# Kernel tuning notes

Hardware: AMD Instinct MI355X
Metric: run time of the kernel (lower is better)

## Reference

```python
import jax, jax.numpy as jnp
import numpy as np

B = 131072      # flattened batch of item embeddings
E = 256         # e_dim; x has 2*E features (src half, rec half)
NQ = 4          # residual quantizer levels per branch
NE = 256        # codebook size per level
BETA = 0.25


def setup_inputs() -> dict:
    key = jax.random.key(0)
    k1, k2, k3 = jax.random.split(key, 3)
    x = jax.random.normal(k1, (B, 2 * E), dtype=jnp.float32)
    src_codebooks = jax.random.normal(k2, (NQ, NE, E), dtype=jnp.float32)
    rec_codebooks = jax.random.normal(k3, (NQ, NE, E), dtype=jnp.float32)
    return {"x": x, "src_codebooks": src_codebooks, "rec_codebooks": rec_codebooks}


def _vq(residual, cb):
    # residual: [B, E], cb: [NE, E]
    # squared euclidean distances via expanded form (GEMM-dominated)
    d = (jnp.sum(residual * residual, axis=1, keepdims=True)
         - 2.0 * (residual @ cb.T)
         + jnp.sum(cb * cb, axis=1)[None, :])          # [B, NE]
    idx = jnp.argmin(d, axis=1)                          # [B]
    x_q = cb[idx]                                        # gather [B, E]
    loss = (jnp.mean((jax.lax.stop_gradient(x_q) - residual) ** 2)
            + BETA * jnp.mean((x_q - jax.lax.stop_gradient(residual)) ** 2))
    # straight-through estimator
    x_q = residual + jax.lax.stop_gradient(x_q - residual)
    return x_q, loss, idx


def _rq(x_part, codebooks):
    # sequential residual VQ chain over NQ levels (small fixed unroll)
    residual = x_part
    x_q = jnp.zeros_like(x_part)
    losses, indices = [], []
    for i in range(codebooks.shape[0]):
        x_res, l, idx = _vq(residual, codebooks[i])
        residual = residual - x_res
        x_q = x_q + x_res
        losses.append(l)
        indices.append(idx)
    return x_q, jnp.stack(losses), jnp.stack(indices, axis=-1)


def reference(x, src_codebooks, rec_codebooks):
    src_x_q, src_l, src_idx = _rq(x[:, :E], src_codebooks)
    rec_x_q, rec_l, rec_idx = _rq(x[:, E:], rec_codebooks)
    mean_loss = jnp.mean(jnp.concatenate([src_l, rec_l]))
    return ((src_x_q, rec_x_q), mean_loss, (src_idx, rec_idx))
```

## Files before the change

### kernel.cpp

```cpp
#include <hip/hip_runtime.h>
#include <hip/hip_bf16.h>
#include <hip/hip_fp16.h>
#include <cstdint>
#include <cstddef>

#define NB   131072
#define ED   256
#define NQL  4
#define NEC  256

typedef _Float16 f16;
typedef f16  f16x8 __attribute__((ext_vector_type(8)));
typedef float f32x4 __attribute__((ext_vector_type(4)));

static constexpr float FMAXV = 3.402823466e+38f;
static constexpr float TAUH  = 0.078125f;

static constexpr size_t OFF_REC  = (size_t)NB * ED;
static constexpr size_t OFF_LOSS = 2 * (size_t)NB * ED;
static constexpr size_t OFF_SIDX = OFF_LOSS + 1;
static constexpr size_t OFF_RIDX = OFF_SIDX + (size_t)NB * NQL;

static constexpr size_t WS_LOSS = 0;
static constexpr size_t WS_NORM = 256;
static constexpr size_t WS_CBH  = 256 + 8 * 256 * 4;

__global__ void kPrep(const float* __restrict__ cbS, const float* __restrict__ cbR,
                      float* __restrict__ norms, double* __restrict__ lossAcc) {
  const int cbi = blockIdx.x;
  const int j   = threadIdx.x;
  if (cbi == 0 && j < 8) lossAcc[j] = 0.0;
  const float* row = (cbi < 4 ? cbS : cbR) + ((size_t)(cbi & 3) * NEC + j) * ED;
  float acc = 0.f;
  for (int k = 0; k < ED; k += 4) {
    float4 v = *(const float4*)(row + k);
    acc += v.x * v.x + v.y * v.y + v.z * v.z + v.w * v.w;
  }
  norms[cbi * NEC + j] = acc - 256.0f;
}

__global__ void kConvH(const float* __restrict__ cbS, const float* __restrict__ cbR,
                       f16* __restrict__ cbH) {
  const int f   = blockIdx.x * 256 + threadIdx.x;
  const int cbi = f >> 16;
  const int rem = f & 65535;
  const float v = (cbi < 4 ? cbS + ((size_t)cbi << 16) : cbR + ((size_t)(cbi - 4) << 16))[rem];
  cbH[f] = (f16)(-v);
}

__device__ __forceinline__ float pk(float v, int j) {
  return __uint_as_float((__float_as_uint(v) & ~255u) | (unsigned)j);
}
__device__ __forceinline__ float unpv(float k) {
  return __uint_as_float(__float_as_uint(k) & ~255u);
}
__device__ __forceinline__ void ins3(float& s0, float& s1, float& s2, float k) {
  float t0 = fmaxf(s0, k); s0 = fminf(s0, k);
  float t1 = fmaxf(s1, t0); s1 = fminf(s1, t0);
  s2 = fminf(s2, t1);
}
__device__ __forceinline__ void mrg3(float& a0, float& a1, float& a2,
                                     float b0, float b1, float b2) {
  float x  = fmaxf(a0, b0);
  float c0 = fminf(a0, b0);
  float m1 = fminf(a1, b1), M1 = fmaxf(a1, b1);
  float c1 = fminf(fminf(x, a1), b1);
  float c2 = fminf(fminf(fmaxf(x, m1), M1), fminf(a2, b2));
  a0 = c0; a1 = c1; a2 = c2;
}

__global__ __launch_bounds__(256, 2)
void kMain(const float* __restrict__ x,
           const float* __restrict__ cbS,
           const float* __restrict__ cbR,
           const f16*  __restrict__ cbH,
           const float* __restrict__ norms,
           double* __restrict__ lossAcc,
           float* __restrict__ out) {
  __shared__ __align__(16) char  RhBuf[64 * 512];
  __shared__ __align__(16) float keybuf[64][4][4];
  __shared__ float redS[4];

  const int tid   = threadIdx.x;
  const int lane  = tid & 63;
  const int w     = tid >> 6;
  const int it_o  = tid >> 2;
  const int kq    = tid & 3;
  const int b0    = blockIdx.x * 64;
  const int br    = blockIdx.y;
  const int l15   = lane & 15;
  const int l4    = lane >> 4;

  const float* cbf32base = br ? cbR : cbS;
  float res[64];
  float lossA = 0.f, lossB = 0.f, lossC = 0.f, lossD = 0.f;

  {
    const float* xp = x + (size_t)(b0 + it_o) * (2 * ED) + br * ED + kq * 64;
#pragma unroll
    for (int i = 0; i < 16; ++i) {
      float4 v = *(const float4*)(xp + 4 * i);
      res[4 * i + 0] = v.x; res[4 * i + 1] = v.y;
      res[4 * i + 2] = v.z; res[4 * i + 3] = v.w;
    }
  }

#pragma unroll 1
  for (int lev = 0; lev < NQL; ++lev) {
    const int cbi = br * 4 + lev;
    const float* nrm = norms + (size_t)cbi * NEC;
    const f16*   cbh = cbH + ((size_t)cbi << 16);
    const float* cbf32 = cbf32base + (size_t)lev * NEC * ED;

#pragma unroll
    for (int c = 0; c < 8; ++c) {
      f16x8 h;
#pragma unroll
      for (int u = 0; u < 8; ++u) h[u] = (f16)res[c * 8 + u];
      int off = it_o * 512 + kq * 128 + c * 16;
      off ^= (it_o & 7) << 4;
      *(f16x8*)&RhBuf[off] = h;
    }

    f32x4 acc[4][4];
#pragma unroll
    for (int nt = 0; nt < 4; ++nt) {
      float4 nv = *(const float4*)&nrm[w * 64 + nt * 16 + l4 * 4];
      f32x4 h; h[0] = 0.5f * nv.x; h[1] = 0.5f * nv.y;
      h[2] = 0.5f * nv.z; h[3] = 0.5f * nv.w;
#pragma unroll
      for (int mt = 0; mt < 4; ++mt) acc[mt][nt] = h;
    }

    f16x8 A0[4], B0[4], A1[4], B1[4];
#define LOADA(Adst, ks_)                                                        \
    {                                                                           \
      _Pragma("unroll")                                                         \
      for (int mt = 0; mt < 4; ++mt) {                                          \
        const int it = mt * 16 + l15;                                           \
        const int offA = (it * 512 + (ks_) * 64 + l4 * 16) ^ ((it & 7) << 4);   \
        Adst[mt] = *(const f16x8*)&RhBuf[offA];                                 \
      }                                                                         \
    }
#define LOADB(Bdst, ks_)                                                        \
    {                                                                           \
      _Pragma("unroll")                                                         \
      for (int nt = 0; nt < 4; ++nt) {                                          \
        const int j = w * 64 + nt * 16 + l15;                                   \
        Bdst[nt] = *(const f16x8*)&cbh[(size_t)j * ED + (ks_) * 32 + l4 * 8];   \
      }                                                                         \
    }
#define MFMA16(Aop, Bop)                                                        \
    {                                                                           \
      __builtin_amdgcn_s_setprio(1);                                            \
      _Pragma("unroll")                                                         \
      for (int mt = 0; mt < 4; ++mt)                                            \
        _Pragma("unroll")                                                       \
        for (int nt = 0; nt < 4; ++nt)                                          \
          acc[mt][nt] = __builtin_amdgcn_mfma_f32_16x16x32_f16(                 \
              Bop[nt], Aop[mt], acc[mt][nt], 0, 0, 0);                          \
      __builtin_amdgcn_s_setprio(0);                                            \
    }

    LOADB(B0, 0);
    __syncthreads();
    LOADA(A0, 0);
#pragma unroll 1
    for (int ks2 = 0; ks2 < 4; ++ks2) {
      LOADA(A1, 2 * ks2 + 1); LOADB(B1, 2 * ks2 + 1);
      MFMA16(A0, B0);
      if (ks2 < 3) { LOADA(A0, 2 * ks2 + 2); LOADB(B0, 2 * ks2 + 2); }
      MFMA16(A1, B1);
    }
#undef LOADA
#undef LOADB
#undef MFMA16

#pragma unroll
    for (int mt = 0; mt < 4; ++mt) {
      float s0 = FMAXV, s1 = FMAXV, s2 = FMAXV;
#pragma unroll
      for (int nt = 0; nt < 4; ++nt)
#pragma unroll
        for (int r = 0; r < 4; ++r)
          ins3(s0, s1, s2, pk(acc[mt][nt][r], w * 64 + nt * 16 + l4 * 4 + r));
      {
        float b0k = __shfl_xor(s0, 16), b1k = __shfl_xor(s1, 16), b2k = __shfl_xor(s2, 16);
        mrg3(s0, s1, s2, b0k, b1k, b2k);
        b0k = __shfl_xor(s0, 32); b1k = __shfl_xor(s1, 32); b2k = __shfl_xor(s2, 32);
        mrg3(s0, s1, s2, b0k, b1k, b2k);
      }
      if (l4 == 0) {
        float4 v; v.x = s0; v.y = s1; v.z = s2; v.w = FMAXV;
        *(float4*)&keybuf[mt * 16 + l15][w][0] = v;
      }
    }
    __syncthreads();

    int jm;
    {
      float4 v = *(const float4*)&keybuf[it_o][kq][0];
      float s0 = v.x, s1 = v.y, s2 = v.z;
      {
        float b0k = __shfl_xor(s0, 1), b1k = __shfl_xor(s1, 1), b2k = __shfl_xor(s2, 1);
        mrg3(s0, s1, s2, b0k, b1k, b2k);
        b0k = __shfl_xor(s0, 2); b1k = __shfl_xor(s1, 2); b2k = __shfl_xor(s2, 2);
        mrg3(s0, s1, s2, b0k, b1k, b2k);
      }
      jm = (int)(__float_as_uint(s0) & 255u);
      const float gap = unpv(s1) - unpv(s0);
      if (gap < TAUH) {
        const int cand[3] = { jm, (int)(__float_as_uint(s1) & 255u),
                                  (int)(__float_as_uint(s2) & 255u) };
        float bestd = FMAXV; int bestj = 0;
#pragma unroll 1
        for (int cc = 0; cc < 3; ++cc) {
          const int j = cand[cc];
          const float* row = cbf32 + (size_t)j * ED + kq * 64;
          float p2 = 0.f;
#pragma unroll
          for (int i = 0; i < 16; ++i) {
            float4 q = *(const float4*)(row + 4 * i);
            p2 = fmaf(res[4 * i + 0], q.x, p2);
            p2 = fmaf(res[4 * i + 1], q.y, p2);
            p2 = fmaf(res[4 * i + 2], q.z, p2);
            p2 = fmaf(res[4 * i + 3], q.w, p2);
          }
          p2 += __shfl_xor(p2, 1);
          p2 += __shfl_xor(p2, 2);
          const float d = fmaf(-2.f, p2, nrm[j]);
          if (d < bestd || (d == bestd && j < bestj)) { bestd = d; bestj = j; }
        }
        jm = bestj;
      }
      if (kq == 0) {
        const size_t ioff = (br ? OFF_RIDX : OFF_SIDX) + (size_t)(b0 + it_o) * NQL + lev;
        out[ioff] = (float)jm;
      }
    }

    {
      const float* crow = cbf32 + (size_t)jm * ED + kq * 64;
#pragma unroll
      for (int i = 0; i < 16; ++i) {
        float4 q = *(const float4*)(crow + 4 * i);
#pragma unroll
        for (int u = 0; u < 4; ++u) {
          float cv = (u == 0 ? q.x : u == 1 ? q.y : u == 2 ? q.z : q.w);
          float r  = res[4 * i + u];
          float dd = cv - r;
          if      (u == 0) lossA = fmaf(dd, dd, lossA);
          else if (u == 1) lossB = fmaf(dd, dd, lossB);
          else if (u == 2) lossC = fmaf(dd, dd, lossC);
          else             lossD = fmaf(dd, dd, lossD);
          float xr = r + dd;
          res[4 * i + u] = r - xr;
        }
      }
    }
  }

  {
    const float* xp = x + (size_t)(b0 + it_o) * (2 * ED) + br * ED + kq * 64;
    float* op = out + (br ? OFF_REC : 0) + (size_t)(b0 + it_o) * ED + kq * 64;
#pragma unroll
    for (int i = 0; i < 16; ++i) {
      float4 xv = *(const float4*)(xp + 4 * i);
      float4 o;
      o.x = xv.x - res[4 * i + 0];
      o.y = xv.y - res[4 * i + 1];
      o.z = xv.z - res[4 * i + 2];
      o.w = xv.w - res[4 * i + 3];
      *(float4*)(op + 4 * i) = o;
    }
  }

  float lossReg = (lossA + lossB) + (lossC + lossD);
#pragma unroll
  for (int d = 1; d < 64; d <<= 1) lossReg += __shfl_xor(lossReg, d);
  if (lane == 0) redS[w] = lossReg;
  __syncthreads();
  if (tid == 0)
    atomicAdd(&lossAcc[blockIdx.x & 7], (double)((redS[0] + redS[1]) + (redS[2] + redS[3])));
}

__global__ void kFin(const double* __restrict__ lossAcc, float* __restrict__ out) {
  if (blockIdx.x == 0 && threadIdx.x == 0) {
    double s = 0.0;
    for (int l = 0; l < 8; ++l) s += lossAcc[l];
    out[OFF_LOSS] = (float)(s * 1.25 / ((double)NB * ED) / 8.0);
  }
}

extern "C" void kernel_launch(void* const* d_in, const int* in_sizes, int n_in,
                              void* d_out, int out_size, void* d_ws, size_t ws_size,
                              hipStream_t stream) {
  const float* x   = (const float*)d_in[0];
  const float* cbS = (const float*)d_in[1];
  const float* cbR = (const float*)d_in[2];
  float* out = (float*)d_out;
  char*  ws  = (char*)d_ws;

  double* lossAcc = (double*)(ws + WS_LOSS);
  float*  norms   = (float*)(ws + WS_NORM);
  f16*    cbH     = (f16*)(ws + WS_CBH);

  hipLaunchKernelGGL(kPrep,  dim3(8),    dim3(256), 0, stream, cbS, cbR, norms, lossAcc);
  hipLaunchKernelGGL(kConvH, dim3(2048), dim3(256), 0, stream, cbS, cbR, cbH);
  hipLaunchKernelGGL(kMain,  dim3(NB / 64, 2), dim3(256), 0, stream,
                     x, cbS, cbR, cbH, norms, lossAcc, out);
  hipLaunchKernelGGL(kFin,   dim3(1),    dim3(64),  0, stream, lossAcc, out);
}
```

Measured before the change: 566.4 us.

## Fuse residual staging into update and prefetch next level's codebook tile

Converts the new residual to f16 and writes it to shared memory inside the residual-update loop, so the separate conversion pass per level goes away. The first B fragment of the next level's codebook is issued right after the argmin sync, so its latency overlaps the index refinement and update. The k-loop is fully unrolled. This adds register pressure and relies on the existing single __syncthreads per level to order the shared-memory writes before the next level's reads.

New measurement: 689.3 us. 21.7% more time.

```diff
diff --git a/kernel.cpp b/kernel.cpp
--- a/kernel.cpp
+++ b/kernel.cpp
@@ -95,44 +95,8 @@
   float res[64];
   float lossA = 0.f, lossB = 0.f, lossC = 0.f, lossD = 0.f;
 
-  {
-    const float* xp = x + (size_t)(b0 + it_o) * (2 * ED) + br * ED + kq * 64;
-#pragma unroll
-    for (int i = 0; i < 16; ++i) {
-      float4 v = *(const float4*)(xp + 4 * i);
-      res[4 * i + 0] = v.x; res[4 * i + 1] = v.y;
-      res[4 * i + 2] = v.z; res[4 * i + 3] = v.w;
-    }
-  }
-
-#pragma unroll 1
-  for (int lev = 0; lev < NQL; ++lev) {
-    const int cbi = br * 4 + lev;
-    const float* nrm = norms + (size_t)cbi * NEC;
-    const f16*   cbh = cbH + ((size_t)cbi << 16);
-    const float* cbf32 = cbf32base + (size_t)lev * NEC * ED;
-
-#pragma unroll
-    for (int c = 0; c < 8; ++c) {
-      f16x8 h;
-#pragma unroll
-      for (int u = 0; u < 8; ++u) h[u] = (f16)res[c * 8 + u];
-      int off = it_o * 512 + kq * 128 + c * 16;
-      off ^= (it_o & 7) << 4;
-      *(f16x8*)&RhBuf[off] = h;
-    }
-
-    f32x4 acc[4][4];
-#pragma unroll
-    for (int nt = 0; nt < 4; ++nt) {
-      float4 nv = *(const float4*)&nrm[w * 64 + nt * 16 + l4 * 4];
-      f32x4 h; h[0] = 0.5f * nv.x; h[1] = 0.5f * nv.y;
-      h[2] = 0.5f * nv.z; h[3] = 0.5f * nv.w;
-#pragma unroll
-      for (int mt = 0; mt < 4; ++mt) acc[mt][nt] = h;
-    }
-
-    f16x8 A0[4], B0[4], A1[4], B1[4];
+  f16x8 A0[4], A1[4], B0[4], B1[4];
+
 #define LOADA(Adst, ks_)                                                        \
     {                                                                           \
       _Pragma("unroll")                                                         \
@@ -142,12 +106,12 @@
         Adst[mt] = *(const f16x8*)&RhBuf[offA];                                 \
       }                                                                         \
     }
-#define LOADB(Bdst, ks_)                                                        \
+#define LOADB(Bdst, ks_, CBH_)                                                  \
     {                                                                           \
       _Pragma("unroll")                                                         \
       for (int nt = 0; nt < 4; ++nt) {                                          \
         const int j = w * 64 + nt * 16 + l15;                                   \
-        Bdst[nt] = *(const f16x8*)&cbh[(size_t)j * ED + (ks_) * 32 + l4 * 8];   \
+        Bdst[nt] = *(const f16x8*)&(CBH_)[(size_t)j * ED + (ks_) * 32 + l4 * 8];\
       }                                                                         \
     }
 #define MFMA16(Aop, Bop)                                                        \
@@ -162,19 +126,54 @@
       __builtin_amdgcn_s_setprio(0);                                            \
     }
 
-    LOADB(B0, 0);
+  {
+    const float* xp = x + (size_t)(b0 + it_o) * (2 * ED) + br * ED + kq * 64;
+#pragma unroll
+    for (int c = 0; c < 8; ++c) {
+      float4 v0 = *(const float4*)(xp + 8 * c);
+      float4 v1 = *(const float4*)(xp + 8 * c + 4);
+      res[8 * c + 0] = v0.x; res[8 * c + 1] = v0.y;
+      res[8 * c + 2] = v0.z; res[8 * c + 3] = v0.w;
+      res[8 * c + 4] = v1.x; res[8 * c + 5] = v1.y;
+      res[8 * c + 6] = v1.z; res[8 * c + 7] = v1.w;
+      f16x8 h;
+      h[0] = (f16)v0.x; h[1] = (f16)v0.y; h[2] = (f16)v0.z; h[3] = (f16)v0.w;
+      h[4] = (f16)v1.x; h[5] = (f16)v1.y; h[6] = (f16)v1.z; h[7] = (f16)v1.w;
+      const int off = (it_o * 512 + kq * 128 + c * 16) ^ ((it_o & 7) << 4);
+      *(f16x8*)&RhBuf[off] = h;
+    }
+  }
+  LOADB(B0, 0, cbH + ((size_t)(br * 4) << 16));
+
+#pragma unroll 1
+  for (int lev = 0; lev < NQL; ++lev) {
+    const int cbi = br * 4 + lev;
+    const float* nrm = norms + (size_t)cbi * NEC;
+    const f16*   cbh = cbH + ((size_t)cbi << 16);
+    const float* cbf32 = cbf32base + (size_t)lev * NEC * ED;
+    const bool doStage = (lev < 3);
+
+    f32x4 acc[4][4];
+#pragma unroll
+    for (int nt = 0; nt < 4; ++nt) {
+      float4 nv = *(const float4*)&nrm[w * 64 + nt * 16 + l4 * 4];
+      f32x4 h; h[0] = 0.5f * nv.x; h[1] = 0.5f * nv.y;
+      h[2] = 0.5f * nv.z; h[3] = 0.5f * nv.w;
+#pragma unroll
+      for (int mt = 0; mt < 4; ++mt) acc[mt][nt] = h;
+    }
+
     __syncthreads();
+
     LOADA(A0, 0);
-#pragma unroll 1
-    for (int ks2 = 0; ks2 < 4; ++ks2) {
-      LOADA(A1, 2 * ks2 + 1); LOADB(B1, 2 * ks2 + 1);
-      MFMA16(A0, B0);
-      if (ks2 < 3) { LOADA(A0, 2 * ks2 + 2); LOADB(B0, 2 * ks2 + 2); }
-      MFMA16(A1, B1);
-    }
-#undef LOADA
-#undef LOADB
-#undef MFMA16
+    LOADA(A1, 1); LOADB(B1, 1, cbh); MFMA16(A0, B0);
+    LOADA(A0, 2); LOADB(B0, 2, cbh); MFMA16(A1, B1);
+    LOADA(A1, 3); LOADB(B1, 3, cbh); MFMA16(A0, B0);
+    LOADA(A0, 4); LOADB(B0, 4, cbh); MFMA16(A1, B1);
+    LOADA(A1, 5); LOADB(B1, 5, cbh); MFMA16(A0, B0);
+    LOADA(A0, 6); LOADB(B0, 6, cbh); MFMA16(A1, B1);
+    LOADA(A1, 7); LOADB(B1, 7, cbh); MFMA16(A0, B0);
+    MFMA16(A1, B1);
 
 #pragma unroll
     for (int mt = 0; mt < 4; ++mt) {
@@ -196,6 +195,8 @@
       }
     }
     __syncthreads();
+
+    if (doStage) LOADB(B0, 0, cbh + (1 << 16));
 
     int jm;
     {
@@ -241,6 +242,7 @@
 
     {
       const float* crow = cbf32 + (size_t)jm * ED + kq * 64;
+      f16x8 h;
 #pragma unroll
       for (int i = 0; i < 16; ++i) {
         float4 q = *(const float4*)(crow + 4 * i);
@@ -254,11 +256,21 @@
           else if (u == 2) lossC = fmaf(dd, dd, lossC);
           else             lossD = fmaf(dd, dd, lossD);
           float xr = r + dd;
-          res[4 * i + u] = r - xr;
+          float rn = r - xr;
+          res[4 * i + u] = rn;
+          h[(i & 1) * 4 + u] = (f16)rn;
         }
-      }
-    }
-  }
+        if (doStage && (i & 1)) {
+          const int c = i >> 1;
+          const int off = (it_o * 512 + kq * 128 + c * 16) ^ ((it_o & 7) << 4);
+          *(f16x8*)&RhBuf[off] = h;
+        }
+      }
+    }
+  }
+#undef LOADA
+#undef LOADB
+#undef MFMA16
 
   {
     const float* xp = x + (size_t)(b0 + it_o) * (2 * ED) + br * ED + kq * 64;
```

## Stage fp16 codebook tiles into LDS via async global_load_lds double buffering

Applied to the files above, without the earlier changes.

Replaces the per-wave direct global loads of the fp16 codebook B fragments with asynchronous global_load_lds copies into a double-buffered LDS staging area, prefetching the next k-step (and the next level's first tile) while the current MFMAs run. B fragments are then read from LDS. The aim is to hide global memory latency and coalesce codebook fetches. In exchange it adds a __syncthreads per k-step, uses 32KB more LDS (which may reduce occupancy with launch_bounds 2), and drops the previous register double buffering.

Measured after the change: 717.4 us. +26.6%, slower.

```diff
diff --git a/kernel.cpp b/kernel.cpp
--- a/kernel.cpp
+++ b/kernel.cpp
@@ -12,6 +12,9 @@
 typedef _Float16 f16;
 typedef f16  f16x8 __attribute__((ext_vector_type(8)));
 typedef float f32x4 __attribute__((ext_vector_type(4)));
+
+typedef const __attribute__((address_space(1))) void* gp1_t;
+typedef __attribute__((address_space(3))) void* lp3_t;
 
 static constexpr float FMAXV = 3.402823466e+38f;
 static constexpr float TAUH  = 0.078125f;
@@ -78,6 +81,7 @@
            double* __restrict__ lossAcc,
            float* __restrict__ out) {
   __shared__ __align__(16) char  RhBuf[64 * 512];
+  __shared__ __align__(16) char  BstgBuf[2 * 16384];
   __shared__ __align__(16) float keybuf[64][4][4];
   __shared__ float redS[4];
 
@@ -95,44 +99,19 @@
   float res[64];
   float lossA = 0.f, lossB = 0.f, lossC = 0.f, lossD = 0.f;
 
-  {
-    const float* xp = x + (size_t)(b0 + it_o) * (2 * ED) + br * ED + kq * 64;
-#pragma unroll
-    for (int i = 0; i < 16; ++i) {
-      float4 v = *(const float4*)(xp + 4 * i);
-      res[4 * i + 0] = v.x; res[4 * i + 1] = v.y;
-      res[4 * i + 2] = v.z; res[4 * i + 3] = v.w;
-    }
-  }
-
-#pragma unroll 1
-  for (int lev = 0; lev < NQL; ++lev) {
-    const int cbi = br * 4 + lev;
-    const float* nrm = norms + (size_t)cbi * NEC;
-    const f16*   cbh = cbH + ((size_t)cbi << 16);
-    const float* cbf32 = cbf32base + (size_t)lev * NEC * ED;
-
-#pragma unroll
-    for (int c = 0; c < 8; ++c) {
-      f16x8 h;
-#pragma unroll
-      for (int u = 0; u < 8; ++u) h[u] = (f16)res[c * 8 + u];
-      int off = it_o * 512 + kq * 128 + c * 16;
-      off ^= (it_o & 7) << 4;
-      *(f16x8*)&RhBuf[off] = h;
-    }
-
-    f32x4 acc[4][4];
-#pragma unroll
-    for (int nt = 0; nt < 4; ++nt) {
-      float4 nv = *(const float4*)&nrm[w * 64 + nt * 16 + l4 * 4];
-      f32x4 h; h[0] = 0.5f * nv.x; h[1] = 0.5f * nv.y;
-      h[2] = 0.5f * nv.z; h[3] = 0.5f * nv.w;
-#pragma unroll
-      for (int mt = 0; mt < 4; ++mt) acc[mt][nt] = h;
-    }
-
-    f16x8 A0[4], B0[4], A1[4], B1[4];
+  f16x8 A0[4];
+
+#define STAGEB(buf_, ks_, CBH_)                                                 \
+    {                                                                           \
+      char* lb = &BstgBuf[(buf_)*16384 + w*4096];                               \
+      const char* gs = (const char*)(CBH_) + (size_t)(ks_)*64 + w*16;           \
+      _Pragma("unroll")                                                         \
+      for (int i2 = 0; i2 < 4; ++i2) {                                          \
+        __builtin_amdgcn_global_load_lds(                                       \
+            (gp1_t)(gs + (size_t)(i2 * 64 + lane) * 512),                       \
+            (lp3_t)(lb + i2 * 1024), 16, 0, 0);                                 \
+      }                                                                         \
+    }
 #define LOADA(Adst, ks_)                                                        \
     {                                                                           \
       _Pragma("unroll")                                                         \
@@ -140,14 +119,6 @@
         const int it = mt * 16 + l15;                                           \
         const int offA = (it * 512 + (ks_) * 64 + l4 * 16) ^ ((it & 7) << 4);   \
         Adst[mt] = *(const f16x8*)&RhBuf[offA];                                 \
-      }                                                                         \
-    }
-#define LOADB(Bdst, ks_)                                                        \
-    {                                                                           \
-      _Pragma("unroll")                                                         \
-      for (int nt = 0; nt < 4; ++nt) {                                          \
-        const int j = w * 64 + nt * 16 + l15;                                   \
-        Bdst[nt] = *(const f16x8*)&cbh[(size_t)j * ED + (ks_) * 32 + l4 * 8];   \
       }                                                                         \
     }
 #define MFMA16(Aop, Bop)                                                        \
@@ -161,20 +132,66 @@
               Bop[nt], Aop[mt], acc[mt][nt], 0, 0, 0);                          \
       __builtin_amdgcn_s_setprio(0);                                            \
     }
-
-    LOADB(B0, 0);
+#define KSTEP(ks_)                                                              \
+    {                                                                           \
+      LOADA(A0, ks_);                                                           \
+      f16x8 Bf[4];                                                              \
+      _Pragma("unroll")                                                         \
+      for (int nt = 0; nt < 4; ++nt) {                                          \
+        const int j = w * 64 + nt * 16 + l15;                                   \
+        Bf[nt] = *(const f16x8*)&BstgBuf[((ks_)&1)*16384 + l4*4096 + j*16];     \
+      }                                                                         \
+      MFMA16(A0, Bf);                                                           \
+    }
+
+  {
+    const float* xp = x + (size_t)(b0 + it_o) * (2 * ED) + br * ED + kq * 64;
+#pragma unroll
+    for (int i = 0; i < 16; ++i) {
+      float4 v = *(const float4*)(xp + 4 * i);
+      res[4 * i + 0] = v.x; res[4 * i + 1] = v.y;
+      res[4 * i + 2] = v.z; res[4 * i + 3] = v.w;
+    }
+  }
+  STAGEB(0, 0, cbH + ((size_t)(br * 4) << 16));
+
+#pragma unroll 1
+  for (int lev = 0; lev < NQL; ++lev) {
+    const int cbi = br * 4 + lev;
+    const float* nrm = norms + (size_t)cbi * NEC;
+    const f16*   cbh = cbH + ((size_t)cbi << 16);
+    const float* cbf32 = cbf32base + (size_t)lev * NEC * ED;
+
+#pragma unroll
+    for (int c = 0; c < 8; ++c) {
+      f16x8 h;
+#pragma unroll
+      for (int u = 0; u < 8; ++u) h[u] = (f16)res[c * 8 + u];
+      int off = it_o * 512 + kq * 128 + c * 16;
+      off ^= (it_o & 7) << 4;
+      *(f16x8*)&RhBuf[off] = h;
+    }
+
+    f32x4 acc[4][4];
+#pragma unroll
+    for (int nt = 0; nt < 4; ++nt) {
+      float4 nv = *(const float4*)&nrm[w * 64 + nt * 16 + l4 * 4];
+      f32x4 h; h[0] = 0.5f * nv.x; h[1] = 0.5f * nv.y;
+      h[2] = 0.5f * nv.z; h[3] = 0.5f * nv.w;
+#pragma unroll
+      for (int mt = 0; mt < 4; ++mt) acc[mt][nt] = h;
+    }
+
     __syncthreads();
-    LOADA(A0, 0);
-#pragma unroll 1
-    for (int ks2 = 0; ks2 < 4; ++ks2) {
-      LOADA(A1, 2 * ks2 + 1); LOADB(B1, 2 * ks2 + 1);
-      MFMA16(A0, B0);
-      if (ks2 < 3) { LOADA(A0, 2 * ks2 + 2); LOADB(B0, 2 * ks2 + 2); }
-      MFMA16(A1, B1);
-    }
-#undef LOADA
-#undef LOADB
-#undef MFMA16
+
+    STAGEB(1, 1, cbh); KSTEP(0); __syncthreads();
+    STAGEB(0, 2, cbh); KSTEP(1); __syncthreads();
+    STAGEB(1, 3, cbh); KSTEP(2); __syncthreads();
+    STAGEB(0, 4, cbh); KSTEP(3); __syncthreads();
+    STAGEB(1, 5, cbh); KSTEP(4); __syncthreads();
+    STAGEB(0, 6, cbh); KSTEP(5); __syncthreads();
+    STAGEB(1, 7, cbh); KSTEP(6); __syncthreads();
+    KSTEP(7);
 
 #pragma unroll
     for (int mt = 0; mt < 4; ++mt) {
@@ -196,6 +213,8 @@
       }
     }
     __syncthreads();
+
+    if (lev < 3) STAGEB(0, 0, cbh + (1 << 16));
 
     int jm;
     {
@@ -259,6 +278,10 @@
       }
     }
   }
+#undef STAGEB
+#undef LOADA
+#undef MFMA16
+#undef KSTEP
 
   {
     const float* xp = x + (size_t)(b0 + it_o) * (2 * ED) + br * ED + kq * 64;
```
